# Optimization experiments

Hardware: AMD Instinct MI355X
Metric: run time of the kernel (lower is better)

Reference implementation:

```python
import jax, jax.numpy as jnp
import numpy as np

B, S, D, H, E = 4, 2048, 256, 8, 65536
HD = D // H  # head_dim = 32


def _layernorm(x, g, b, eps=1e-5):
    mu = jnp.mean(x, axis=-1, keepdims=True)
    var = jnp.var(x, axis=-1, keepdims=True)
    return (x - mu) * jax.lax.rsqrt(var + eps) * g + b


def setup_inputs() -> dict:
    key = jax.random.key(0)
    ks = jax.random.split(key, 16)
    sd = 1.0 / np.sqrt(D)
    inp = {
        "x": jax.random.normal(ks[0], (B, S, D), jnp.float32),
        "adj_mask": jax.random.uniform(ks[1], (B, S, S)) < 0.05,  # ~32 neighbors/node
        "edge_attr": jax.random.normal(ks[2], (E,), jnp.float32),
        "edge_index": jax.random.randint(ks[3], (2, E), 0, S),
        "ln1_g": jnp.ones((D,), jnp.float32),
        "ln1_b": jnp.zeros((D,), jnp.float32),
        "wq": jax.random.normal(ks[4], (D, D), jnp.float32) * sd,
        "bq": jnp.zeros((D,), jnp.float32),
        "wk": jax.random.normal(ks[5], (D, D), jnp.float32) * sd,
        "bk": jnp.zeros((D,), jnp.float32),
        "wv": jax.random.normal(ks[6], (D, D), jnp.float32) * sd,
        "bv": jnp.zeros((D,), jnp.float32),
        "wo": jax.random.normal(ks[7], (D, D), jnp.float32) * sd,
        "bo": jnp.zeros((D,), jnp.float32),
        "ln2_g": jnp.ones((D,), jnp.float32),
        "ln2_b": jnp.zeros((D,), jnp.float32),
        "w1": jax.random.normal(ks[8], (4 * D, D), jnp.float32) * sd,
        "b1": jnp.zeros((4 * D,), jnp.float32),
        "w2": jax.random.normal(ks[9], (D, 4 * D), jnp.float32) * (1.0 / np.sqrt(4 * D)),
        "b2": jnp.zeros((D,), jnp.float32),
    }
    return inp


def reference(x, adj_mask, edge_attr, edge_index,
              ln1_g, ln1_b, wq, bq, wk, bk, wv, bv, wo, bo,
              ln2_g, ln2_b, w1, b1, w2, b2):
    residual = x
    nx = _layernorm(x, ln1_g, ln1_b)
    # projections (torch Linear: y = x W^T + b)
    q = nx @ wq.T + bq
    k = nx @ wk.T + bk
    v = nx @ wv.T + bv
    # (B,S,D) -> (B,H,S,HD)
    q = q.reshape(B, S, H, HD).transpose(0, 2, 1, 3)
    k = k.reshape(B, S, H, HD).transpose(0, 2, 1, 3)
    v = v.reshape(B, S, H, HD).transpose(0, 2, 1, 3)
    scores = jnp.einsum("bhqd,bhkd->bhqk", q, k) / np.sqrt(HD)
    scores = jnp.where(adj_mask[:, None, :, :], scores, -1e9)
    # edge-attr bias: scatter clipped attr into (S,S), gated per-batch by adj_mask,
    # broadcast over heads (replaces the nested python loop)
    clipped = jnp.clip(edge_attr, -5.0, 5.0)
    bias2d = jnp.zeros((S, S), scores.dtype).at[edge_index[0], edge_index[1]].set(clipped)
    scores = scores + jnp.where(adj_mask, bias2d[None, :, :], 0.0)[:, None, :, :]
    attn = jax.nn.softmax(scores, axis=-1)
    ctx = jnp.einsum("bhqk,bhkd->bhqd", attn, v)
    ctx = ctx.transpose(0, 2, 1, 3).reshape(B, S, D)
    x = residual + (ctx @ wo.T + bo)
    # MLP block (exact GELU, like torch nn.GELU())
    n2 = _layernorm(x, ln2_g, ln2_b)
    h = jax.nn.gelu(n2 @ w1.T + b1, approximate=False)
    x = x + (h @ w2.T + b2)
    return x
```

## Files before the change

### kernel.cpp

```cpp
#include <hip/hip_runtime.h>
#include <stdint.h>

#define S 2048
#define D 256
#define H 8
#define HD 32
#define E_EDGES 65536
#define DFF 1024
#define M_TOK 8192
#define CAP 512

typedef __attribute__((ext_vector_type(8))) short s16x8;
typedef __attribute__((ext_vector_type(8))) unsigned short u16x8;
typedef __attribute__((ext_vector_type(4))) float f32x4;

__device__ __forceinline__ float b2f(unsigned short u){
  union { unsigned int i; float f; } x; x.i = ((unsigned int)u) << 16; return x.f;
}
__device__ __forceinline__ unsigned short f2b(float f){
  union { float f; unsigned int i; } x; x.f = f;
  unsigned int r = x.i + 0x7fffu + ((x.i >> 16) & 1u);
  return (unsigned short)(r >> 16);
}

__global__ __launch_bounds__(256) void cvt_kernel(
    const float* __restrict__ in, unsigned short* __restrict__ out, int n4)
{
  int i = blockIdx.x * 256 + threadIdx.x;
  if (i >= n4) return;
  const float4 v = *(const float4*)(in + (size_t)i * 4);
  unsigned short o[4] = { f2b(v.x), f2b(v.y), f2b(v.z), f2b(v.w) };
  *(uint2*)(out + (size_t)i * 4) = *(const uint2*)o;
}

__global__ __launch_bounds__(256) void ln_kernel(
    const float* __restrict__ xf,
    const float* __restrict__ g, const float* __restrict__ bt,
    unsigned short* __restrict__ out)
{
  const int wave = threadIdx.x >> 6;
  const int lane = threadIdx.x & 63;
  const int row = blockIdx.x * 4 + wave;
  const size_t base = (size_t)row * D + lane * 4;
  const float4 u = *(const float4*)(xf + base);
  float v[4] = { u.x, u.y, u.z, u.w };
  float s  = v[0]+v[1]+v[2]+v[3];
  float s2 = v[0]*v[0]+v[1]*v[1]+v[2]*v[2]+v[3]*v[3];
  #pragma unroll
  for (int off=32; off>=1; off>>=1){ s += __shfl_xor(s,off,64); s2 += __shfl_xor(s2,off,64); }
  const float mu  = s * (1.f/D);
  const float var = s2 * (1.f/D) - mu*mu;
  const float rs  = 1.f / sqrtf(var + 1e-5f);
  #pragma unroll
  for (int j=0;j<4;++j){
    const int c = lane*4 + j;
    const float y = (v[j]-mu)*rs*g[c] + bt[c];
    out[(size_t)row*D + c] = f2b(y);
  }
}

__global__ __launch_bounds__(256) void gemm_kernel(
    const unsigned short* __restrict__ A,
    const unsigned short* __restrict__ W,
    const float* __restrict__ bias,
    unsigned short* __restrict__ outb,
    float* __restrict__ outf,
    const float* __restrict__ resf,
    int M, int N, int K, int act)
{
  __shared__ unsigned short As[64][40];
  __shared__ unsigned short Bs[64][40];
  const int tid  = threadIdx.x;
  const int wave = tid >> 6;
  const int lane = tid & 63;
  const int m0 = blockIdx.y * 64;
  const int n0 = blockIdx.x * 64;
  const int srow = tid >> 2;
  const int scol = (tid & 3) * 8;
  const int fr = lane & 15;
  const int kf = (lane >> 4) * 8;
  f32x4 acc[4];
  #pragma unroll
  for (int i=0;i<4;++i)
    #pragma unroll
    for (int r=0;r<4;++r) acc[i][r] = 0.f;

  for (int k0 = 0; k0 < K; k0 += 32) {
    *(u16x8*)&As[srow][scol] = *(const u16x8*)(A + (size_t)(m0+srow)*K + k0 + scol);
    *(u16x8*)&Bs[srow][scol] = *(const u16x8*)(W + (size_t)(n0+srow)*K + k0 + scol);
    __syncthreads();
    s16x8 bfrag = *(const s16x8*)&Bs[wave*16 + fr][kf];
    #pragma unroll
    for (int i = 0; i < 4; ++i) {
      s16x8 afrag = *(const s16x8*)&As[i*16 + fr][kf];
      acc[i] = __builtin_amdgcn_mfma_f32_16x16x32_bf16(afrag, bfrag, acc[i], 0, 0, 0);
    }
    __syncthreads();
  }
  const int col = n0 + wave*16 + fr;
  const float bvl = bias[col];
  const int rbase = (lane >> 4) * 4;
  #pragma unroll
  for (int i = 0; i < 4; ++i) {
    #pragma unroll
    for (int r = 0; r < 4; ++r) {
      const int row = m0 + i*16 + rbase + r;
      const size_t off = (size_t)row * N + col;
      float vv = acc[i][r] + bvl;
      if (act) vv = 0.5f * vv * (1.0f + erff(vv * 0.70710678118654752f));
      if (resf) vv += resf[off];
      if (outb) outb[off] = f2b(vv);
      if (outf) outf[off] = vv;
    }
  }
}

__global__ __launch_bounds__(256) void zero_kernel(uint4* __restrict__ p, int n4) {
  int i = blockIdx.x * 256 + threadIdx.x;
  if (i < n4) { uint4 z; z.x=0; z.y=0; z.z=0; z.w=0; p[i] = z; }
}
__global__ __launch_bounds__(256) void scatter_kernel(
    const int* __restrict__ ei, const float* __restrict__ attr,
    unsigned int* __restrict__ packed)
{
  int e = blockIdx.x * 256 + threadIdx.x;
  if (e >= E_EDGES) return;
  int r = ei[e], c = ei[E_EDGES + e];
  float v = attr[e];
  v = fminf(5.f, fmaxf(-5.f, v));
  unsigned int pk = (((unsigned int)e) << 16) | (unsigned int)f2b(v);
  atomicMax(&packed[(size_t)r * S + c], pk);
}

__global__ __launch_bounds__(256) void attn_kernel(
    const unsigned short* __restrict__ qg,
    const unsigned short* __restrict__ kg,
    const unsigned short* __restrict__ vg,
    const int* __restrict__ mask,
    const unsigned int* __restrict__ packed,
    unsigned short* __restrict__ ctx)
{
  __shared__ unsigned short nidx[CAP];
  __shared__ float nbias[CAP];
  __shared__ float sc[H*CAP];
  __shared__ float qs[D];
  __shared__ int wtot[4], wbase[4], cnt_s;
  const int t = threadIdx.x;
  const int wave = t >> 6, lane = t & 63;
  const int bqi = blockIdx.x;
  const int b = bqi >> 11;
  const int qrow = bqi & (S-1);
  qs[t] = b2f(qg[(size_t)bqi * D + t]);

  const int* mrow = mask + (size_t)bqi * S;
  const uint4 ma = *(const uint4*)(mrow + t*8);
  const uint4 mb = *(const uint4*)(mrow + t*8 + 4);
  unsigned int mv[8] = { ma.x, ma.y, ma.z, ma.w, mb.x, mb.y, mb.z, mb.w };
  int mycnt = 0;
  #pragma unroll
  for (int j = 0; j < 8; ++j) mycnt += mv[j] ? 1 : 0;
  int inc = mycnt;
  #pragma unroll
  for (int off=1; off<64; off<<=1){ int y = __shfl_up(inc, off, 64); if (lane >= off) inc += y; }
  if (lane == 63) wtot[wave] = inc;
  __syncthreads();
  if (t == 0) { int ss=0; for (int w=0; w<4; ++w){ wbase[w]=ss; ss+=wtot[w]; } cnt_s = ss; }
  __syncthreads();
  int pos = wbase[wave] + inc - mycnt;
  #pragma unroll
  for (int j = 0; j < 8; ++j) {
    if (mv[j]) {
      if (pos < CAP) nidx[pos] = (unsigned short)(t*8 + j);
      ++pos;
    }
  }
  __syncthreads();
  int cnt = cnt_s; if (cnt > CAP) cnt = CAP;

  for (int i = t; i < cnt; i += 256) {
    unsigned int pkv = packed[(size_t)qrow * S + nidx[i]];
    nbias[i] = b2f((unsigned short)(pkv & 0xffffu));
  }
  __syncthreads();

  const float scale = 0.17677669529663687f;
  for (int i = t; i < cnt*H; i += 256) {
    const int h = i & 7, n = i >> 3;
    const int nk = nidx[n];
    const unsigned short* krow = kg + ((size_t)(b*S + nk))*D + h*HD;
    float sdot = 0.f;
    #pragma unroll
    for (int c4 = 0; c4 < 4; ++c4) {
      u16x8 kv = *(const u16x8*)(krow + c4*8);
      #pragma unroll
      for (int j = 0; j < 8; ++j) sdot += qs[h*HD + c4*8 + j] * b2f(kv[j]);
    }
    sc[h*CAP + n] = sdot * scale + nbias[n];
  }
  __syncthreads();

  const int h = t >> 5, dd = t & 31;
  float outv;
  if (cnt > 0) {
    float m = -1e30f;
    for (int n = dd; n < cnt; n += 32) m = fmaxf(m, sc[h*CAP + n]);
    #pragma unroll
    for (int off=16; off>=1; off>>=1) m = fmaxf(m, __shfl_xor(m, off, 64));
    float sum = 0.f;
    for (int n = dd; n < cnt; n += 32) {
      float e = __expf(sc[h*CAP + n] - m);
      sc[h*CAP + n] = e;
      sum += e;
    }
    #pragma unroll
    for (int off=16; off>=1; off>>=1) sum += __shfl_xor(sum, off, 64);
    __syncthreads();
    float a = 0.f;
    const unsigned short* vbase = vg + (size_t)b*S*D + h*HD + dd;
    for (int n = 0; n < cnt; ++n)
      a += sc[h*CAP + n] * b2f(vbase[(size_t)nidx[n] * D]);
    outv = a / sum;
  } else {
    float a = 0.f;
    const unsigned short* vbase = vg + (size_t)b*S*D + h*HD + dd;
    for (int n = 0; n < S; ++n) a += b2f(vbase[(size_t)n * D]);
    outv = a * (1.f / S);
  }
  ctx[(size_t)bqi * D + t] = f2b(outv);
}

extern "C" void kernel_launch(void* const* d_in, const int* in_sizes, int n_in,
                              void* d_out, int out_size, void* d_ws, size_t ws_size,
                              hipStream_t stream) {
  const float*          x    = (const float*)d_in[0];
  const int*            mask = (const int*)d_in[1];
  const float*          eat  = (const float*)d_in[2];
  const int*            eidx = (const int*)d_in[3];
  const float*          ln1g = (const float*)d_in[4];
  const float*          ln1b = (const float*)d_in[5];
  const float*          wq   = (const float*)d_in[6];
  const float*          bq   = (const float*)d_in[7];
  const float*          wk   = (const float*)d_in[8];
  const float*          bk   = (const float*)d_in[9];
  const float*          wv   = (const float*)d_in[10];
  const float*          bv   = (const float*)d_in[11];
  const float*          wo   = (const float*)d_in[12];
  const float*          bo   = (const float*)d_in[13];
  const float*          ln2g = (const float*)d_in[14];
  const float*          ln2b = (const float*)d_in[15];
  const float*          w1   = (const float*)d_in[16];
  const float*          b1   = (const float*)d_in[17];
  const float*          w2   = (const float*)d_in[18];
  const float*          b2   = (const float*)d_in[19];
  float* out = (float*)d_out;

  char* ws = (char*)d_ws;
  unsigned short* nx  = (unsigned short*)ws;
  unsigned short* qb  = nx + (size_t)M_TOK*D;
  unsigned short* kbf = qb + (size_t)M_TOK*D;
  unsigned short* vbf = kbf + (size_t)M_TOK*D;
  unsigned short* cx  = vbf + (size_t)M_TOK*D;
  float*          x1  = (float*)(cx + (size_t)M_TOK*D);
  unsigned int*   pk  = (unsigned int*)(x1 + (size_t)M_TOK*D);
  unsigned short* wqb = (unsigned short*)(pk + (size_t)S*S);
  unsigned short* wkb = wqb + (size_t)D*D;
  unsigned short* wvb = wkb + (size_t)D*D;
  unsigned short* wob = wvb + (size_t)D*D;
  unsigned short* w1b = wob + (size_t)D*D;
  unsigned short* w2b = w1b + (size_t)DFF*D;
  unsigned short* hb  = qb;
  unsigned short* n2  = nx;

  cvt_kernel<<<D*D/4/256,   256, 0, stream>>>(wq, wqb, D*D/4);
  cvt_kernel<<<D*D/4/256,   256, 0, stream>>>(wk, wkb, D*D/4);
  cvt_kernel<<<D*D/4/256,   256, 0, stream>>>(wv, wvb, D*D/4);
  cvt_kernel<<<D*D/4/256,   256, 0, stream>>>(wo, wob, D*D/4);
  cvt_kernel<<<DFF*D/4/256, 256, 0, stream>>>(w1, w1b, DFF*D/4);
  cvt_kernel<<<DFF*D/4/256, 256, 0, stream>>>(w2, w2b, DFF*D/4);

  zero_kernel<<<(S*S/4 + 255)/256, 256, 0, stream>>>((uint4*)pk, S*S/4);
  scatter_kernel<<<E_EDGES/256, 256, 0, stream>>>(eidx, eat, pk);
  ln_kernel<<<M_TOK/4, 256, 0, stream>>>(x, ln1g, ln1b, nx);
  gemm_kernel<<<dim3(D/64,  M_TOK/64), 256, 0, stream>>>(nx, wqb, bq, qb, nullptr, nullptr, M_TOK, D, D, 0);
  gemm_kernel<<<dim3(D/64,  M_TOK/64), 256, 0, stream>>>(nx, wkb, bk, kbf, nullptr, nullptr, M_TOK, D, D, 0);
  gemm_kernel<<<dim3(D/64,  M_TOK/64), 256, 0, stream>>>(nx, wvb, bv, vbf, nullptr, nullptr, M_TOK, D, D, 0);
  attn_kernel<<<M_TOK, 256, 0, stream>>>(qb, kbf, vbf, mask, pk, cx);
  gemm_kernel<<<dim3(D/64,  M_TOK/64), 256, 0, stream>>>(cx, wob, bo, nullptr, x1, x, M_TOK, D, D, 0);
  ln_kernel<<<M_TOK/4, 256, 0, stream>>>(x1, ln2g, ln2b, n2);
  gemm_kernel<<<dim3(DFF/64, M_TOK/64), 256, 0, stream>>>(n2, w1b, b1, hb, nullptr, nullptr, M_TOK, DFF, D, 1);
  gemm_kernel<<<dim3(D/64,  M_TOK/64), 256, 0, stream>>>(hb, w2b, b2, nullptr, out, x1, M_TOK, D, DFF, 0);
}
```

Before: 184.1 us.

## Fuse QKV projections, template GEMM tiles, restructure attention score layout

Merges the Q, K and V projections into one GEMM over a concatenated 768-wide weight and bias, writing an interleaved QKV buffer that attention reads with a row stride of 768. The GEMM becomes a template with 2x2 wave tiling and larger 128x128 or 128x64 block tiles, so each wave issues several MFMAs per LDS fragment load. Attention now keeps the query head slice in registers, stores scores as [neighbor][head] with a padded stride of 9, and drops one barrier. The gain sought is fewer launches, more operand reuse in the GEMMs and fewer LDS reads in the score loop, at the cost of higher register pressure and strided K/V row accesses.

```diff
diff --git a/kernel.cpp b/kernel.cpp
--- a/kernel.cpp
+++ b/kernel.cpp
@@ -9,6 +9,7 @@
 #define DFF 1024
 #define M_TOK 8192
 #define CAP 512
+#define QKVN 768
 
 typedef __attribute__((ext_vector_type(8))) short s16x8;
 typedef __attribute__((ext_vector_type(8))) unsigned short u16x8;
@@ -59,7 +60,8 @@
   }
 }
 
-__global__ __launch_bounds__(256) void gemm_kernel(
+template<int BM, int BN>
+__global__ __launch_bounds__(256) void gemm_tile(
     const unsigned short* __restrict__ A,
     const unsigned short* __restrict__ W,
     const float* __restrict__ bias,
@@ -68,49 +70,65 @@
     const float* __restrict__ resf,
     int M, int N, int K, int act)
 {
-  __shared__ unsigned short As[64][40];
-  __shared__ unsigned short Bs[64][40];
+  constexpr int WM = BM / 2, WN = BN / 2;
+  constexpr int MI = WM / 16, NI = WN / 16;
+  __shared__ unsigned short As[BM][40];
+  __shared__ unsigned short Bs[BN][40];
   const int tid  = threadIdx.x;
   const int wave = tid >> 6;
   const int lane = tid & 63;
-  const int m0 = blockIdx.y * 64;
-  const int n0 = blockIdx.x * 64;
+  const int wr = wave >> 1, wc = wave & 1;
+  const int m0 = blockIdx.y * BM;
+  const int n0 = blockIdx.x * BN;
   const int srow = tid >> 2;
   const int scol = (tid & 3) * 8;
   const int fr = lane & 15;
   const int kf = (lane >> 4) * 8;
-  f32x4 acc[4];
-  #pragma unroll
-  for (int i=0;i<4;++i)
-    #pragma unroll
-    for (int r=0;r<4;++r) acc[i][r] = 0.f;
+  f32x4 acc[MI][NI];
+  #pragma unroll
+  for (int i=0;i<MI;++i)
+    #pragma unroll
+    for (int j=0;j<NI;++j)
+      #pragma unroll
+      for (int r=0;r<4;++r) acc[i][j][r] = 0.f;
 
   for (int k0 = 0; k0 < K; k0 += 32) {
-    *(u16x8*)&As[srow][scol] = *(const u16x8*)(A + (size_t)(m0+srow)*K + k0 + scol);
-    *(u16x8*)&Bs[srow][scol] = *(const u16x8*)(W + (size_t)(n0+srow)*K + k0 + scol);
+    #pragma unroll
+    for (int rr = 0; rr < BM; rr += 64)
+      *(u16x8*)&As[srow+rr][scol] = *(const u16x8*)(A + (size_t)(m0+srow+rr)*K + k0 + scol);
+    #pragma unroll
+    for (int rr = 0; rr < BN; rr += 64)
+      *(u16x8*)&Bs[srow+rr][scol] = *(const u16x8*)(W + (size_t)(n0+srow+rr)*K + k0 + scol);
     __syncthreads();
-    s16x8 bfrag = *(const s16x8*)&Bs[wave*16 + fr][kf];
-    #pragma unroll
-    for (int i = 0; i < 4; ++i) {
-      s16x8 afrag = *(const s16x8*)&As[i*16 + fr][kf];
-      acc[i] = __builtin_amdgcn_mfma_f32_16x16x32_bf16(afrag, bfrag, acc[i], 0, 0, 0);
-    }
+    s16x8 af[MI], bf[NI];
+    #pragma unroll
+    for (int i = 0; i < MI; ++i) af[i] = *(const s16x8*)&As[wr*WM + i*16 + fr][kf];
+    #pragma unroll
+    for (int j = 0; j < NI; ++j) bf[j] = *(const s16x8*)&Bs[wc*WN + j*16 + fr][kf];
+    #pragma unroll
+    for (int i = 0; i < MI; ++i)
+      #pragma unroll
+      for (int j = 0; j < NI; ++j)
+        acc[i][j] = __builtin_amdgcn_mfma_f32_16x16x32_bf16(af[i], bf[j], acc[i][j], 0, 0, 0);
     __syncthreads();
   }
-  const int col = n0 + wave*16 + fr;
-  const float bvl = bias[col];
   const int rbase = (lane >> 4) * 4;
   #pragma unroll
-  for (int i = 0; i < 4; ++i) {
-    #pragma unroll
-    for (int r = 0; r < 4; ++r) {
-      const int row = m0 + i*16 + rbase + r;
-      const size_t off = (size_t)row * N + col;
-      float vv = acc[i][r] + bvl;
-      if (act) vv = 0.5f * vv * (1.0f + erff(vv * 0.70710678118654752f));
-      if (resf) vv += resf[off];
-      if (outb) outb[off] = f2b(vv);
-      if (outf) outf[off] = vv;
+  for (int j = 0; j < NI; ++j) {
+    const int col = n0 + wc*WN + j*16 + fr;
+    const float bvl = bias[col];
+    #pragma unroll
+    for (int i = 0; i < MI; ++i) {
+      #pragma unroll
+      for (int r = 0; r < 4; ++r) {
+        const int row = m0 + wr*WM + i*16 + rbase + r;
+        const size_t off = (size_t)row * N + col;
+        float vv = acc[i][j][r] + bvl;
+        if (act) vv = 0.5f * vv * (1.0f + erff(vv * 0.70710678118654752f));
+        if (resf) vv += resf[off];
+        if (outb) outb[off] = f2b(vv);
+        if (outf) outf[off] = vv;
+      }
     }
   }
 }
@@ -133,16 +151,14 @@
 }
 
 __global__ __launch_bounds__(256) void attn_kernel(
-    const unsigned short* __restrict__ qg,
-    const unsigned short* __restrict__ kg,
-    const unsigned short* __restrict__ vg,
+    const unsigned short* __restrict__ qkv,
     const int* __restrict__ mask,
     const unsigned int* __restrict__ packed,
     unsigned short* __restrict__ ctx)
 {
   __shared__ unsigned short nidx[CAP];
   __shared__ float nbias[CAP];
-  __shared__ float sc[H*CAP];
+  __shared__ float sc[CAP*9];
   __shared__ float qs[D];
   __shared__ int wtot[4], wbase[4], cnt_s;
   const int t = threadIdx.x;
@@ -150,7 +166,7 @@
   const int bqi = blockIdx.x;
   const int b = bqi >> 11;
   const int qrow = bqi & (S-1);
-  qs[t] = b2f(qg[(size_t)bqi * D + t]);
+  qs[t] = b2f(qkv[(size_t)bqi * QKVN + t]);
 
   const int* mrow = mask + (size_t)bqi * S;
   const uint4 ma = *(const uint4*)(mrow + t*8);
@@ -184,18 +200,23 @@
   __syncthreads();
 
   const float scale = 0.17677669529663687f;
-  for (int i = t; i < cnt*H; i += 256) {
-    const int h = i & 7, n = i >> 3;
-    const int nk = nidx[n];
-    const unsigned short* krow = kg + ((size_t)(b*S + nk))*D + h*HD;
-    float sdot = 0.f;
-    #pragma unroll
-    for (int c4 = 0; c4 < 4; ++c4) {
-      u16x8 kv = *(const u16x8*)(krow + c4*8);
+  {
+    const int h8 = t & 7;
+    float qreg[32];
+    #pragma unroll
+    for (int j = 0; j < 32; ++j) qreg[j] = qs[h8*HD + j];
+    const size_t kbase = (size_t)b * S * QKVN + 256 + h8*HD;
+    for (int n = (t >> 3); n < cnt; n += 32) {
+      const unsigned short* krow = qkv + kbase + (size_t)nidx[n] * QKVN;
+      float sdot = 0.f;
       #pragma unroll
-      for (int j = 0; j < 8; ++j) sdot += qs[h*HD + c4*8 + j] * b2f(kv[j]);
+      for (int c4 = 0; c4 < 4; ++c4) {
+        u16x8 kv = *(const u16x8*)(krow + c4*8);
+        #pragma unroll
+        for (int j = 0; j < 8; ++j) sdot += qreg[c4*8 + j] * b2f(kv[j]);
+      }
+      sc[n*9 + h8] = sdot * scale + nbias[n];
     }
-    sc[h*CAP + n] = sdot * scale + nbias[n];
   }
   __syncthreads();
 
@@ -203,27 +224,26 @@
   float outv;
   if (cnt > 0) {
     float m = -1e30f;
-    for (int n = dd; n < cnt; n += 32) m = fmaxf(m, sc[h*CAP + n]);
+    for (int n = dd; n < cnt; n += 32) m = fmaxf(m, sc[n*9 + h]);
     #pragma unroll
     for (int off=16; off>=1; off>>=1) m = fmaxf(m, __shfl_xor(m, off, 64));
     float sum = 0.f;
     for (int n = dd; n < cnt; n += 32) {
-      float e = __expf(sc[h*CAP + n] - m);
-      sc[h*CAP + n] = e;
+      float e = __expf(sc[n*9 + h] - m);
+      sc[n*9 + h] = e;
       sum += e;
     }
     #pragma unroll
     for (int off=16; off>=1; off>>=1) sum += __shfl_xor(sum, off, 64);
-    __syncthreads();
     float a = 0.f;
-    const unsigned short* vbase = vg + (size_t)b*S*D + h*HD + dd;
+    const unsigned short* vbase = qkv + (size_t)b*S*QKVN + 512 + h*HD + dd;
     for (int n = 0; n < cnt; ++n)
-      a += sc[h*CAP + n] * b2f(vbase[(size_t)nidx[n] * D]);
+      a += sc[n*9 + h] * b2f(vbase[(size_t)nidx[n] * QKVN]);
     outv = a / sum;
   } else {
     float a = 0.f;
-    const unsigned short* vbase = vg + (size_t)b*S*D + h*HD + dd;
-    for (int n = 0; n < S; ++n) a += b2f(vbase[(size_t)n * D]);
+    const unsigned short* vbase = qkv + (size_t)b*S*QKVN + 512 + h*HD + dd;
+    for (int n = 0; n < S; ++n) a += b2f(vbase[(size_t)n * QKVN]);
     outv = a * (1.f / S);
   }
   ctx[(size_t)bqi * D + t] = f2b(outv);
@@ -255,38 +275,36 @@
   float* out = (float*)d_out;
 
   char* ws = (char*)d_ws;
-  unsigned short* nx  = (unsigned short*)ws;
-  unsigned short* qb  = nx + (size_t)M_TOK*D;
-  unsigned short* kbf = qb + (size_t)M_TOK*D;
-  unsigned short* vbf = kbf + (size_t)M_TOK*D;
-  unsigned short* cx  = vbf + (size_t)M_TOK*D;
-  float*          x1  = (float*)(cx + (size_t)M_TOK*D);
-  unsigned int*   pk  = (unsigned int*)(x1 + (size_t)M_TOK*D);
-  unsigned short* wqb = (unsigned short*)(pk + (size_t)S*S);
-  unsigned short* wkb = wqb + (size_t)D*D;
-  unsigned short* wvb = wkb + (size_t)D*D;
-  unsigned short* wob = wvb + (size_t)D*D;
-  unsigned short* w1b = wob + (size_t)D*D;
-  unsigned short* w2b = w1b + (size_t)DFF*D;
-  unsigned short* hb  = qb;
-  unsigned short* n2  = nx;
-
-  cvt_kernel<<<D*D/4/256,   256, 0, stream>>>(wq, wqb, D*D/4);
-  cvt_kernel<<<D*D/4/256,   256, 0, stream>>>(wk, wkb, D*D/4);
-  cvt_kernel<<<D*D/4/256,   256, 0, stream>>>(wv, wvb, D*D/4);
+  unsigned short* nx   = (unsigned short*)ws;
+  unsigned short* qkv  = nx + (size_t)M_TOK*D;
+  unsigned short* cx   = qkv + (size_t)M_TOK*QKVN;
+  float*          x1   = (float*)(cx + (size_t)M_TOK*D);
+  unsigned int*   pk   = (unsigned int*)(x1 + (size_t)M_TOK*D);
+  unsigned short* wqkvb= (unsigned short*)(pk + (size_t)S*S);
+  unsigned short* wob  = wqkvb + (size_t)QKVN*D;
+  unsigned short* w1b  = wob + (size_t)D*D;
+  unsigned short* w2b  = w1b + (size_t)DFF*D;
+  float*          bqkv = (float*)(w2b + (size_t)D*DFF);
+  unsigned short* hb   = qkv;
+  unsigned short* n2   = nx;
+
+  cvt_kernel<<<D*D/4/256,   256, 0, stream>>>(wq, wqkvb,             D*D/4);
+  cvt_kernel<<<D*D/4/256,   256, 0, stream>>>(wk, wqkvb + (size_t)D*D,   D*D/4);
+  cvt_kernel<<<D*D/4/256,   256, 0, stream>>>(wv, wqkvb + (size_t)2*D*D, D*D/4);
   cvt_kernel<<<D*D/4/256,   256, 0, stream>>>(wo, wob, D*D/4);
   cvt_kernel<<<DFF*D/4/256, 256, 0, stream>>>(w1, w1b, DFF*D/4);
   cvt_kernel<<<DFF*D/4/256, 256, 0, stream>>>(w2, w2b, DFF*D/4);
+  hipMemcpyAsync(bqkv,       bq, D*sizeof(float), hipMemcpyDeviceToDevice, stream);
+  hipMemcpyAsync(bqkv + D,   bk, D*sizeof(float), hipMemcpyDeviceToDevice, stream);
+  hipMemcpyAsync(bqkv + 2*D, bv, D*sizeof(float), hipMemcpyDeviceToDevice, stream);
 
   zero_kernel<<<(S*S/4 + 255)/256, 256, 0, stream>>>((uint4*)pk, S*S/4);
   scatter_kernel<<<E_EDGES/256, 256, 0, stream>>>(eidx, eat, pk);
   ln_kernel<<<M_TOK/4, 256, 0, stream>>>(x, ln1g, ln1b, nx);
-  gemm_kernel<<<dim3(D/64,  M_TOK/64), 256, 0, stream>>>(nx, wqb, bq, qb, nullptr, nullptr, M_TOK, D, D, 0);
-  gemm_kernel<<<dim3(D/64,  M_TOK/64), 256, 0, stream>>>(nx, wkb, bk, kbf, nullptr, nullptr, M_TOK, D, D, 0);
-  gemm_kernel<<<dim3(D/64,  M_TOK/64), 256, 0, stream>>>(nx, wvb, bv, vbf, nullptr, nullptr, M_TOK, D, D, 0);
-  attn_kernel<<<M_TOK, 256, 0, stream>>>(qb, kbf, vbf, mask, pk, cx);
-  gemm_kernel<<<dim3(D/64,  M_TOK/64), 256, 0, stream>>>(cx, wob, bo, nullptr, x1, x, M_TOK, D, D, 0);
+  gemm_tile<128,128><<<dim3(QKVN/128, M_TOK/128), 256, 0, stream>>>(nx, wqkvb, bqkv, qkv, nullptr, nullptr, M_TOK, QKVN, D, 0);
+  attn_kernel<<<M_TOK, 256, 0, stream>>>(qkv, mask, pk, cx);
+  gemm_tile<128,64><<<dim3(D/64, M_TOK/128), 256, 0, stream>>>(cx, wob, bo, nullptr, x1, x, M_TOK, D, D, 0);
   ln_kernel<<<M_TOK/4, 256, 0, stream>>>(x1, ln2g, ln2b, n2);
-  gemm_kernel<<<dim3(DFF/64, M_TOK/64), 256, 0, stream>>>(n2, w1b, b1, hb, nullptr, nullptr, M_TOK, DFF, D, 1);
-  gemm_kernel<<<dim3(D/64,  M_TOK/64), 256, 0, stream>>>(hb, w2b, b2, nullptr, out, x1, M_TOK, D, DFF, 0);
-}
+  gemm_tile<128,128><<<dim3(DFF/128, M_TOK/128), 256, 0, stream>>>(n2, w1b, b1, hb, nullptr, nullptr, M_TOK, DFF, D, 1);
+  gemm_tile<128,64><<<dim3(D/64, M_TOK/128), 256, 0, stream>>>(hb, w2b, b2, nullptr, out, x1, M_TOK, D, DFF, 0);
+}
```

Result: slower. 209.8 us (+14.0%).
